# Kernel optimization log

Hardware: AMD Instinct MI355X
Metric: run time of the kernel (lower is better)

Reference implementation:

```python
import jax, jax.numpy as jnp
import numpy as np


def setup_inputs() -> dict:
    key = jax.random.key(0)
    ks = jax.random.split(key, 10)
    B, D_X, D_H, D_S, D_T = 16384, 256, 512, 128, 128
    G = 4 * D_H
    sc = lambda d: 1.0 / np.sqrt(d)
    return {
        "x": jax.random.normal(ks[0], (B, D_X), jnp.float32),
        "h": jax.random.normal(ks[1], (B, D_H), jnp.float32),
        "c": jax.random.normal(ks[2], (B, D_H), jnp.float32),
        "spatial_per_step": jax.random.normal(ks[3], (B, D_S), jnp.float32),
        "temporal_per_step": jax.random.normal(ks[4], (B, D_T), jnp.float32),
        "W_x": jax.random.normal(ks[5], (D_X, G), jnp.float32) * sc(D_X),
        "W_h": jax.random.normal(ks[6], (D_H, G), jnp.float32) * sc(D_H),
        "b_h": jax.random.normal(ks[7], (G,), jnp.float32) * 0.01,
        "W_s": jax.random.normal(ks[8], (D_S, G), jnp.float32) * sc(D_S),
        "W_t": jax.random.normal(ks[9], (D_T, G), jnp.float32) * sc(D_T),
    }


def reference(x, h, c, spatial_per_step, temporal_per_step, W_x, W_h, b_h, W_s, W_t):
    H = W_h.shape[0]  # hidden_size
    # Four gate projections summed (the fusion opportunity): [B, 4H]
    preact = (x @ W_x) + (h @ W_h + b_h) + (spatial_per_step @ W_s) + (temporal_per_step @ W_t)
    i_g = jax.nn.sigmoid(preact[:, 0 * H:1 * H])
    f_g = jax.nn.sigmoid(preact[:, 1 * H:2 * H])
    o_g = jax.nn.sigmoid(preact[:, 2 * H:3 * H])
    c_g = jnp.tanh(preact[:, 3 * H:4 * H])
    c_new = f_g * c + i_g * c_g
    # NOTE: faithful to the source, h = tanh(o * c) (not o * tanh(c))
    h_new = jnp.tanh(o_g * c_new)
    return (h_new, c_new)
```

## Files before the change

### kernel.cpp

```cpp
#include <hip/hip_runtime.h>
#include <hip/hip_bf16.h>
#include <cstdint>

#define B_DIM 16384
#define DX 256
#define DH 512
#define DS 128
#define DT 128
#define KDIM 1024
#define NDIM 2048
#define HOUT 512

typedef __attribute__((ext_vector_type(8))) short short8;
typedef __attribute__((ext_vector_type(4))) float floatx4;

union bf16x8 {
  short8 v;
  __hip_bfloat16 b[8];
};

__device__ __forceinline__ float fast_sigmoid(float x) {
  return 1.f / (1.f + __expf(-x));
}
__device__ __forceinline__ float fast_tanh(float x) {
  float e = __expf(-2.f * x);
  return (1.f - e) / (1.f + e);
}

__global__ __launch_bounds__(256) void pack_A(
    const float* __restrict__ x, const float* __restrict__ h,
    const float* __restrict__ s, const float* __restrict__ t,
    __hip_bfloat16* __restrict__ Ap) {
  int tid = blockIdx.x * 256 + threadIdx.x;
  int b = tid >> 7;
  int k = (tid & 127) * 8;
  const float* p;
  if (k < 256)      p = x + (size_t)b * DX + k;
  else if (k < 768) p = h + (size_t)b * DH + (k - 256);
  else if (k < 896) p = s + (size_t)b * DS + (k - 768);
  else              p = t + (size_t)b * DT + (k - 896);
  floatx4 v0 = *(const floatx4*)p;
  floatx4 v1 = *(const floatx4*)(p + 4);
  bf16x8 o;
#pragma unroll
  for (int j = 0; j < 4; ++j) {
    o.b[j]     = __float2bfloat16(v0[j]);
    o.b[4 + j] = __float2bfloat16(v1[j]);
  }
  *(short8*)(Ap + (size_t)b * KDIM + k) = o.v;
}

__global__ __launch_bounds__(256) void pack_W(
    const float* __restrict__ Wx, const float* __restrict__ Wh,
    const float* __restrict__ Ws, const float* __restrict__ Wt,
    __hip_bfloat16* __restrict__ Wp) {
  int t = blockIdx.x * 256 + threadIdx.x;
  int n = t & (NDIM - 1);
  int k0 = (t >> 11) * 8;
  int g = (n >> 5) & 3, nb = n >> 7, hl = n & 31;
  int c = g * 512 + nb * 32 + hl;
  const float* src; int kl;
  if (k0 < 256)      { src = Wx; kl = k0; }
  else if (k0 < 768) { src = Wh; kl = k0 - 256; }
  else if (k0 < 896) { src = Ws; kl = k0 - 768; }
  else               { src = Wt; kl = k0 - 896; }
  bf16x8 o;
#pragma unroll
  for (int r = 0; r < 8; ++r)
    o.b[r] = __float2bfloat16(src[(size_t)(kl + r) * NDIM + c]);
  *(short8*)(Wp + (size_t)n * KDIM + k0) = o.v;
}

__global__ __launch_bounds__(256, 4) void lstm_gemm(
    const __hip_bfloat16* __restrict__ Ap, const __hip_bfloat16* __restrict__ Wp,
    const float* __restrict__ bh, const float* __restrict__ c_in,
    float* __restrict__ out) {
  __shared__ unsigned short As[128 * 32];
  __shared__ unsigned short Bs[128 * 32];

  const int tid = threadIdx.x;
  const int lane = tid & 63;
  const int wid = tid >> 6;
  const int q = lane >> 4;
  const int fr = lane & 15;
  const int fk = q * 8;
  const int m0 = blockIdx.y * 128;
  const int nb = blockIdx.x;
  const int n0 = nb * 128;
  const int hg0 = nb * 32;

  floatx4 acc[2][8];
#pragma unroll
  for (int i = 0; i < 2; ++i)
#pragma unroll
    for (int j = 0; j < 8; ++j) acc[i][j] = (floatx4)0.f;

  const int ldrow = lane >> 2;
  const int ldk = (lane & 3) * 8;

  for (int kt = 0; kt < KDIM; kt += 32) {
#pragma unroll
    for (int j = 0; j < 2; ++j) {
      const int chunk = wid * 2 + j;
      const int row = chunk * 16 + ldrow;
      const __hip_bfloat16* ga = Ap + (size_t)(m0 + row) * KDIM + kt + ldk;
      __builtin_amdgcn_global_load_lds(
          (const __attribute__((address_space(1))) void*)ga,
          (__attribute__((address_space(3))) void*)&As[chunk * 512], 16, 0, 0);
      const __hip_bfloat16* gb = Wp + (size_t)(n0 + row) * KDIM + kt + ldk;
      __builtin_amdgcn_global_load_lds(
          (const __attribute__((address_space(1))) void*)gb,
          (__attribute__((address_space(3))) void*)&Bs[chunk * 512], 16, 0, 0);
    }
    __syncthreads();

    short8 af[2];
#pragma unroll
    for (int mi = 0; mi < 2; ++mi)
      af[mi] = *(const short8*)&As[(wid * 32 + mi * 16 + fr) * 32 + fk];
#pragma unroll
    for (int half = 0; half < 2; ++half) {
      short8 bf[4];
#pragma unroll
      for (int ni = 0; ni < 4; ++ni)
        bf[ni] = *(const short8*)&Bs[((half * 4 + ni) * 16 + fr) * 32 + fk];
#pragma unroll
      for (int mi = 0; mi < 2; ++mi)
#pragma unroll
        for (int ni = 0; ni < 4; ++ni)
          acc[mi][half * 4 + ni] = __builtin_amdgcn_mfma_f32_16x16x32_bf16(
              af[mi], bf[ni], acc[mi][half * 4 + ni], 0, 0, 0);
    }
    __syncthreads();
  }

  float bias[2][4];
#pragma unroll
  for (int hb = 0; hb < 2; ++hb) {
    const int hh = hg0 + hb * 16 + fr;
#pragma unroll
    for (int g = 0; g < 4; ++g) bias[hb][g] = bh[g * 512 + hh];
  }

#pragma unroll
  for (int mi = 0; mi < 2; ++mi) {
    const int rowl = wid * 32 + mi * 16 + q * 4;
#pragma unroll
    for (int r = 0; r < 4; ++r) {
      const size_t grow = (size_t)(m0 + rowl + r);
#pragma unroll
      for (int hb = 0; hb < 2; ++hb) {
        const int hh = hg0 + hb * 16 + fr;
        const float pi = acc[mi][0 + hb][r] + bias[hb][0];
        const float pf = acc[mi][2 + hb][r] + bias[hb][1];
        const float po = acc[mi][4 + hb][r] + bias[hb][2];
        const float pc = acc[mi][6 + hb][r] + bias[hb][3];
        const float ig = fast_sigmoid(pi);
        const float fg = fast_sigmoid(pf);
        const float og = fast_sigmoid(po);
        const float cg = fast_tanh(pc);
        const float cc = fg * c_in[grow * HOUT + hh] + ig * cg;
        out[grow * HOUT + hh] = fast_tanh(og * cc);
        out[(size_t)B_DIM * HOUT + grow * HOUT + hh] = cc;
      }
    }
  }
}

extern "C" void kernel_launch(void* const* d_in, const int* in_sizes, int n_in,
                              void* d_out, int out_size, void* d_ws, size_t ws_size,
                              hipStream_t stream) {
  const float* x  = (const float*)d_in[0];
  const float* h  = (const float*)d_in[1];
  const float* c  = (const float*)d_in[2];
  const float* sp = (const float*)d_in[3];
  const float* tp = (const float*)d_in[4];
  const float* Wx = (const float*)d_in[5];
  const float* Wh = (const float*)d_in[6];
  const float* bh = (const float*)d_in[7];
  const float* Ws = (const float*)d_in[8];
  const float* Wt = (const float*)d_in[9];
  float* out = (float*)d_out;

  __hip_bfloat16* Ap = (__hip_bfloat16*)d_ws;
  __hip_bfloat16* Wp = (__hip_bfloat16*)((char*)d_ws + (size_t)B_DIM * KDIM * 2);

  pack_A<<<dim3(B_DIM * KDIM / 8 / 256), dim3(256), 0, stream>>>(x, h, sp, tp, Ap);
  pack_W<<<dim3(NDIM * 128 / 256), dim3(256), 0, stream>>>(Wx, Wh, Ws, Wt, Wp);
  lstm_gemm<<<dim3(NDIM / 128, B_DIM / 128), dim3(256), 0, stream>>>(Ap, Wp, bh, c, out);
}
```

Baseline: 256.6 us.

## Pre-tile A and W into MFMA-ready blocks, load B fragments directly to registers

The pack kernels now write A and W in a tiled layout, with 128x64 tiles split into 16-row chunks laid out contiguously. The GEMM then streams A tiles into LDS with fully contiguous global_load_lds. B fragments are read straight from global memory into registers, so the B shared buffer goes away. The K step grows from 32 to 64, the warp layout changes to 2x2 with 64x16-per-gate tiles, and the occupancy hint drops from 4 to 3. This cuts the number of LDS round trips and barriers per K step, at the cost of uncached-by-LDS global reads for B and more register pressure.

```diff
diff --git a/kernel.cpp b/kernel.cpp
--- a/kernel.cpp
+++ b/kernel.cpp
@@ -27,13 +27,19 @@
   return (1.f - e) / (1.f + e);
 }
 
+
 __global__ __launch_bounds__(256) void pack_A(
     const float* __restrict__ x, const float* __restrict__ h,
     const float* __restrict__ s, const float* __restrict__ t,
     __hip_bfloat16* __restrict__ Ap) {
   int tid = blockIdx.x * 256 + threadIdx.x;
-  int b = tid >> 7;
-  int k = (tid & 127) * 8;
+  int i = tid & 63;
+  int tt = (tid >> 6) & 15;
+  int tile = tid >> 10;
+  int kb = tile & 15, mb = tile >> 4;
+  int sp = tt >> 3, c = tt & 7;
+  int b = mb * 128 + c * 16 + (i >> 2);
+  int k = kb * 64 + sp * 32 + (i & 3) * 8;
   const float* p;
   if (k < 256)      p = x + (size_t)b * DX + k;
   else if (k < 768) p = h + (size_t)b * DH + (k - 256);
@@ -47,122 +53,118 @@
     o.b[j]     = __float2bfloat16(v0[j]);
     o.b[4 + j] = __float2bfloat16(v1[j]);
   }
-  *(short8*)(Ap + (size_t)b * KDIM + k) = o.v;
+  *(short8*)(Ap + (size_t)tid * 8) = o.v;
 }
 
 __global__ __launch_bounds__(256) void pack_W(
     const float* __restrict__ Wx, const float* __restrict__ Wh,
     const float* __restrict__ Ws, const float* __restrict__ Wt,
     __hip_bfloat16* __restrict__ Wp) {
-  int t = blockIdx.x * 256 + threadIdx.x;
-  int n = t & (NDIM - 1);
-  int k0 = (t >> 11) * 8;
-  int g = (n >> 5) & 3, nb = n >> 7, hl = n & 31;
-  int c = g * 512 + nb * 32 + hl;
+  int tid = blockIdx.x * 256 + threadIdx.x;
+  int i = tid & 63;
+  int tt = (tid >> 6) & 15;
+  int tile = tid >> 10;
+  int kb = tile & 15, nblk = tile >> 4;
+  int sp = tt >> 3, c = tt & 7;
+  int nl = c * 16 + (i >> 2);
+  int k = kb * 64 + sp * 32 + (i & 3) * 8;
+  int wn = nl >> 6, g = (nl >> 4) & 3, hl = nl & 15;
+  int col = g * 512 + nblk * 32 + wn * 16 + hl;
   const float* src; int kl;
-  if (k0 < 256)      { src = Wx; kl = k0; }
-  else if (k0 < 768) { src = Wh; kl = k0 - 256; }
-  else if (k0 < 896) { src = Ws; kl = k0 - 768; }
-  else               { src = Wt; kl = k0 - 896; }
+  if (k < 256)      { src = Wx; kl = k; }
+  else if (k < 768) { src = Wh; kl = k - 256; }
+  else if (k < 896) { src = Ws; kl = k - 768; }
+  else              { src = Wt; kl = k - 896; }
   bf16x8 o;
 #pragma unroll
   for (int r = 0; r < 8; ++r)
-    o.b[r] = __float2bfloat16(src[(size_t)(kl + r) * NDIM + c]);
-  *(short8*)(Wp + (size_t)n * KDIM + k0) = o.v;
+    o.b[r] = __float2bfloat16(src[(size_t)(kl + r) * NDIM + col]);
+  *(short8*)(Wp + (size_t)tid * 8) = o.v;
 }
 
-__global__ __launch_bounds__(256, 4) void lstm_gemm(
+__global__ __launch_bounds__(256, 3) void lstm_gemm(
     const __hip_bfloat16* __restrict__ Ap, const __hip_bfloat16* __restrict__ Wp,
     const float* __restrict__ bh, const float* __restrict__ c_in,
     float* __restrict__ out) {
-  __shared__ unsigned short As[128 * 32];
-  __shared__ unsigned short Bs[128 * 32];
+  __shared__ unsigned short As[2 * 128 * 32];
 
   const int tid = threadIdx.x;
   const int lane = tid & 63;
   const int wid = tid >> 6;
+  const int wm = wid & 1;
+  const int wn = wid >> 1;
   const int q = lane >> 4;
   const int fr = lane & 15;
-  const int fk = q * 8;
-  const int m0 = blockIdx.y * 128;
-  const int nb = blockIdx.x;
-  const int n0 = nb * 128;
-  const int hg0 = nb * 32;
+  const int mb = blockIdx.y;
+  const int nblk = blockIdx.x;
+  const int m0 = mb * 128;
 
-  floatx4 acc[2][8];
+  floatx4 acc[4][4];
 #pragma unroll
-  for (int i = 0; i < 2; ++i)
+  for (int i = 0; i < 4; ++i)
 #pragma unroll
-    for (int j = 0; j < 8; ++j) acc[i][j] = (floatx4)0.f;
+    for (int j = 0; j < 4; ++j) acc[i][j] = (floatx4)0.f;
 
-  const int ldrow = lane >> 2;
-  const int ldk = (lane & 3) * 8;
+  const int blane = (fr * 4 + q) * 8;
 
-  for (int kt = 0; kt < KDIM; kt += 32) {
+  for (int kt = 0; kt < KDIM / 64; ++kt) {
+    const size_t abase = ((size_t)(mb * 16 + kt) * 16) * 512;
 #pragma unroll
-    for (int j = 0; j < 2; ++j) {
-      const int chunk = wid * 2 + j;
-      const int row = chunk * 16 + ldrow;
-      const __hip_bfloat16* ga = Ap + (size_t)(m0 + row) * KDIM + kt + ldk;
+    for (int j = 0; j < 4; ++j) {
+      const int chunk = wid * 4 + j;
       __builtin_amdgcn_global_load_lds(
-          (const __attribute__((address_space(1))) void*)ga,
+          (const __attribute__((address_space(1))) void*)
+              (Ap + abase + (size_t)chunk * 512 + lane * 8),
           (__attribute__((address_space(3))) void*)&As[chunk * 512], 16, 0, 0);
-      const __hip_bfloat16* gb = Wp + (size_t)(n0 + row) * KDIM + kt + ldk;
-      __builtin_amdgcn_global_load_lds(
-          (const __attribute__((address_space(1))) void*)gb,
-          (__attribute__((address_space(3))) void*)&Bs[chunk * 512], 16, 0, 0);
     }
+    short8 bf[2][4];
+    const size_t bbase = ((size_t)(nblk * 16 + kt) * 16) * 512;
+#pragma unroll
+    for (int sp = 0; sp < 2; ++sp)
+#pragma unroll
+      for (int ni = 0; ni < 4; ++ni)
+        bf[sp][ni] = *(const short8*)(Wp + bbase +
+                         (size_t)(sp * 8 + wn * 4 + ni) * 512 + blane);
     __syncthreads();
 
-    short8 af[2];
 #pragma unroll
-    for (int mi = 0; mi < 2; ++mi)
-      af[mi] = *(const short8*)&As[(wid * 32 + mi * 16 + fr) * 32 + fk];
+    for (int sp = 0; sp < 2; ++sp) {
+      short8 af[4];
 #pragma unroll
-    for (int half = 0; half < 2; ++half) {
-      short8 bf[4];
+      for (int mi = 0; mi < 4; ++mi)
+        af[mi] = *(const short8*)&As[sp * 4096 +
+                                     (wm * 64 + mi * 16 + fr) * 32 + q * 8];
 #pragma unroll
-      for (int ni = 0; ni < 4; ++ni)
-        bf[ni] = *(const short8*)&Bs[((half * 4 + ni) * 16 + fr) * 32 + fk];
-#pragma unroll
-      for (int mi = 0; mi < 2; ++mi)
+      for (int mi = 0; mi < 4; ++mi)
 #pragma unroll
         for (int ni = 0; ni < 4; ++ni)
-          acc[mi][half * 4 + ni] = __builtin_amdgcn_mfma_f32_16x16x32_bf16(
-              af[mi], bf[ni], acc[mi][half * 4 + ni], 0, 0, 0);
+          acc[mi][ni] = __builtin_amdgcn_mfma_f32_16x16x32_bf16(
+              af[mi], bf[sp][ni], acc[mi][ni], 0, 0, 0);
     }
     __syncthreads();
   }
 
-  float bias[2][4];
+  const int hh = nblk * 32 + wn * 16 + fr;
+  float bias[4];
 #pragma unroll
-  for (int hb = 0; hb < 2; ++hb) {
-    const int hh = hg0 + hb * 16 + fr;
-#pragma unroll
-    for (int g = 0; g < 4; ++g) bias[hb][g] = bh[g * 512 + hh];
-  }
+  for (int g = 0; g < 4; ++g) bias[g] = bh[g * 512 + hh];
 
 #pragma unroll
-  for (int mi = 0; mi < 2; ++mi) {
-    const int rowl = wid * 32 + mi * 16 + q * 4;
+  for (int mi = 0; mi < 4; ++mi) {
 #pragma unroll
     for (int r = 0; r < 4; ++r) {
-      const size_t grow = (size_t)(m0 + rowl + r);
-#pragma unroll
-      for (int hb = 0; hb < 2; ++hb) {
-        const int hh = hg0 + hb * 16 + fr;
-        const float pi = acc[mi][0 + hb][r] + bias[hb][0];
-        const float pf = acc[mi][2 + hb][r] + bias[hb][1];
-        const float po = acc[mi][4 + hb][r] + bias[hb][2];
-        const float pc = acc[mi][6 + hb][r] + bias[hb][3];
-        const float ig = fast_sigmoid(pi);
-        const float fg = fast_sigmoid(pf);
-        const float og = fast_sigmoid(po);
-        const float cg = fast_tanh(pc);
-        const float cc = fg * c_in[grow * HOUT + hh] + ig * cg;
-        out[grow * HOUT + hh] = fast_tanh(og * cc);
-        out[(size_t)B_DIM * HOUT + grow * HOUT + hh] = cc;
-      }
+      const size_t grow = (size_t)(m0 + wm * 64 + mi * 16 + q * 4 + r);
+      const float pi = acc[mi][0][r] + bias[0];
+      const float pf = acc[mi][1][r] + bias[1];
+      const float po = acc[mi][2][r] + bias[2];
+      const float pc = acc[mi][3][r] + bias[3];
+      const float ig = fast_sigmoid(pi);
+      const float fg = fast_sigmoid(pf);
+      const float og = fast_sigmoid(po);
+      const float cg = fast_tanh(pc);
+      const float cc = fg * c_in[grow * HOUT + hh] + ig * cg;
+      out[grow * HOUT + hh] = fast_tanh(og * cc);
+      out[(size_t)B_DIM * HOUT + grow * HOUT + hh] = cc;
     }
   }
 }
@@ -186,6 +188,6 @@
   __hip_bfloat16* Wp = (__hip_bfloat16*)((char*)d_ws + (size_t)B_DIM * KDIM * 2);
 
   pack_A<<<dim3(B_DIM * KDIM / 8 / 256), dim3(256), 0, stream>>>(x, h, sp, tp, Ap);
-  pack_W<<<dim3(NDIM * 128 / 256), dim3(256), 0, stream>>>(Wx, Wh, Ws, Wt, Wp);
+  pack_W<<<dim3(NDIM * KDIM / 8 / 256), dim3(256), 0, stream>>>(Wx, Wh, Ws, Wt, Wp);
   lstm_gemm<<<dim3(NDIM / 128, B_DIM / 128), dim3(256), 0, stream>>>(Ap, Wp, bh, c, out);
 }
```

New measurement: 251.4 us. -2.0%, faster.
